# Performance work log

Measured on AMD Instinct MI355X. Metric: run time of the kernel, lower is better.

Reference implementation:

```python
import jax, jax.numpy as jnp
import numpy as np

B, S, D, H = 1, 4096, 1024, 16
HD = D // H  # 64
THETA = 10000.0


def precompute_freqs_cis(dim, end, theta=THETA):
    freqs = 1.0 / theta ** (np.arange(0, dim, 2, dtype=np.float32) / dim)  # [dim//2]
    t = np.arange(end, dtype=np.float32)
    f = np.outer(t, freqs)                       # [end, dim//2]
    f = np.concatenate((f, f), axis=-1)          # [end, dim]
    return jnp.asarray(np.cos(f), jnp.float32), jnp.asarray(np.sin(f), jnp.float32)


def rotate_half(x):
    x1 = x[..., : x.shape[-1] // 2]
    x2 = x[..., x.shape[-1] // 2:]
    return jnp.concatenate((-x2, x1), axis=-1)


def setup_inputs() -> dict:
    key = jax.random.key(0)
    ks = jax.random.split(key, 5)
    x = jax.random.normal(ks[0], (B, S, D), jnp.float32)
    scale = 0.02
    Wq = jax.random.normal(ks[1], (D, H, HD), jnp.float32) * scale
    Wk = jax.random.normal(ks[2], (D, H, HD), jnp.float32) * scale
    Wv = jax.random.normal(ks[3], (D, H, HD), jnp.float32) * scale
    Wo = jax.random.normal(ks[4], (H, HD, D), jnp.float32) * scale
    mask = jnp.tril(jnp.ones((S, S), jnp.bool_))[None, None]  # [1,1,S,S] causal
    return {"x": x, "mask": mask, "Wq": Wq, "Wk": Wk, "Wv": Wv, "Wo": Wo}


def reference(x, mask, Wq, Wk, Wv, Wo):
    # QKV projections: [B,S,D] x [D,H,HD] -> [B,S,H,HD]
    q = jnp.einsum('bsd,dhe->bshe', x, Wq)
    k = jnp.einsum('bsd,dhe->bshe', x, Wk)
    v = jnp.einsum('bsd,dhe->bshe', x, Wv)
    # Rotary position embedding
    cos, sin = precompute_freqs_cis(HD, S)
    cos = cos[None, :, None, :]  # [1,S,1,HD]
    sin = sin[None, :, None, :]
    q = q * cos + rotate_half(q) * sin
    k = k * cos + rotate_half(k) * sin
    # Scaled dot-product attention
    scale = 1.0 / jnp.sqrt(jnp.asarray(HD, jnp.float32))
    scores = jnp.einsum('bqhe,bkhe->bhqk', q * scale, k)  # [B,H,S,S]
    big_neg = jnp.finfo(scores.dtype).min
    scores = jnp.where(mask, scores, big_neg)
    attn = jax.nn.softmax(scores, axis=-1)
    ctx = jnp.einsum('bhqk,bkhe->bqhe', attn, v)  # [B,S,H,HD]
    # Output projection contracting (head, head_dim)
    out = jnp.einsum('bqhe,hed->bqd', ctx, Wo)  # [B,S,D]
    return out
```

## Files before the change

### kernel.cpp

```cpp
#include <hip/hip_runtime.h>
#include <hip/hip_bf16.h>
#include <stdint.h>
#include <stddef.h>

#define S_LEN 4096
#define DMODEL 1024
#define NHEAD 16
#define HDIM 64
#define L2E 1.4426950408889634f
#define FIXED_M 8.0f

typedef __attribute__((ext_vector_type(8))) short bf16x8;
typedef __attribute__((ext_vector_type(8))) unsigned short u16x8;
typedef __attribute__((ext_vector_type(4))) float f32x4;
typedef __attribute__((ext_vector_type(16))) float f32x16;

__device__ __forceinline__ unsigned short f2bf(float f) {
    unsigned int u = __float_as_uint(f);
    return (unsigned short)((u + 0x7FFFu + ((u >> 16) & 1u)) >> 16);
}
__device__ __forceinline__ float bf2f(unsigned short h) {
    return __uint_as_float(((unsigned int)h) << 16);
}

__device__ __forceinline__ void gload_lds16(const unsigned short* g, unsigned short* l) {
    __builtin_amdgcn_global_load_lds(
        (const __attribute__((address_space(1))) unsigned int*)g,
        (__attribute__((address_space(3))) unsigned int*)l, 16, 0, 0);
}

__global__ __launch_bounds__(256) void rope_table_kernel(float* __restrict__ ctab,
                                                         float* __restrict__ stab) {
    int i = blockIdx.x * 256 + threadIdx.x;
    int s = i >> 5, j = i & 31;
    float freq = exp2f(-0.41524101186092407f * (float)j);
    float ang = (float)s * freq;
    ctab[i] = cosf(ang);
    stab[i] = sinf(ang);
}

__global__ __launch_bounds__(256) void cvt_x_kernel(const float* __restrict__ x,
                                                    unsigned short* __restrict__ xb) {
    int i = (blockIdx.x * 256 + threadIdx.x) * 8;
    f32x4 a = *(const f32x4*)(x + i);
    f32x4 b = *(const f32x4*)(x + i + 4);
    u16x8 o;
    #pragma unroll
    for (int j = 0; j < 4; ++j) { o[j] = f2bf(a[j]); o[4 + j] = f2bf(b[j]); }
    *(u16x8*)(xb + i) = o;
}

__global__ __launch_bounds__(256) void cvt_wt_kernel(
    const float* __restrict__ w0, const float* __restrict__ w1,
    const float* __restrict__ w2, const float* __restrict__ w3,
    unsigned short* __restrict__ t0, unsigned short* __restrict__ t1,
    unsigned short* __restrict__ t2, unsigned short* __restrict__ t3) {
    const float* src; unsigned short* dst;
    switch (blockIdx.z) {
        case 0: src = w0; dst = t0; break;
        case 1: src = w1; dst = t1; break;
        case 2: src = w2; dst = t2; break;
        default: src = w3; dst = t3; break;
    }
    __shared__ float tile[64][65];
    int t = threadIdx.x;
    int k0 = blockIdx.y * 64, n0 = blockIdx.x * 64;
    int r = t >> 2, q4 = (t & 3) * 16;
    const float* sp = src + (size_t)(k0 + r) * DMODEL + n0 + q4;
    #pragma unroll
    for (int j = 0; j < 4; ++j) {
        f32x4 v = *(const f32x4*)(sp + j * 4);
        #pragma unroll
        for (int e = 0; e < 4; ++e) tile[r][q4 + j * 4 + e] = v[e];
    }
    __syncthreads();
    int n = t >> 2, kq = (t & 3) * 16;
    unsigned short* dp = dst + (size_t)(n0 + n) * DMODEL + k0 + kq;
    u16x8 a, b;
    #pragma unroll
    for (int j = 0; j < 8; ++j) { a[j] = f2bf(tile[kq + j][n]); b[j] = f2bf(tile[kq + 8 + j][n]); }
    *(u16x8*)dp = a;
    *(u16x8*)(dp + 8) = b;
}

template<int MODE>
__global__ __launch_bounds__(256) void gemm_kernel(
    const unsigned short* __restrict__ Ab,
    const unsigned short* __restrict__ B0,
    const unsigned short* __restrict__ B1,
    const unsigned short* __restrict__ B2,
    unsigned short* __restrict__ o0,
    unsigned short* __restrict__ o1,
    unsigned short* __restrict__ o2,
    float* __restrict__ fo,
    const float* __restrict__ ctab,
    const float* __restrict__ stab) {
    int z = blockIdx.z;
    const unsigned short* Bt = (MODE == 0) ? B0 : (z == 0 ? B0 : (z == 1 ? B1 : B2));
    unsigned short* outp     = (MODE == 0) ? o0 : (z == 0 ? o0 : (z == 1 ? o1 : o2));
    int m0 = blockIdx.y * 128, n0 = blockIdx.x * 128;
    __shared__ unsigned short As[128][64];
    __shared__ unsigned short Bs[128][64];
    int t = threadIdx.x, w = t >> 6, l = t & 63;
    int wm = w >> 1, wn = w & 1, g = l >> 4, c = l & 15;

    f32x4 acc[4][4];
    #pragma unroll
    for (int m = 0; m < 4; ++m)
        #pragma unroll
        for (int n = 0; n < 4; ++n) acc[m][n] = (f32x4){0.f, 0.f, 0.f, 0.f};

    int srow = l >> 3;
    int scol = (l & 7) * 8;

    for (int kt = 0; kt < DMODEL; kt += 64) {
        __syncthreads();
        #pragma unroll
        for (int ch = 0; ch < 4; ++ch) {
            int chunk = w + ch * 4;
            gload_lds16(Ab + (size_t)(m0 + chunk * 8 + srow) * DMODEL + kt + scol,
                        (unsigned short*)As + chunk * 512);
            gload_lds16(Bt + (size_t)(n0 + chunk * 8 + srow) * DMODEL + kt + scol,
                        (unsigned short*)Bs + chunk * 512);
        }
        __syncthreads();
        #pragma unroll
        for (int kk = 0; kk < 64; kk += 32) {
            bf16x8 af[4], bf[4];
            #pragma unroll
            for (int m = 0; m < 4; ++m) af[m] = *(const bf16x8*)&As[wm * 64 + m * 16 + c][kk + g * 8];
            #pragma unroll
            for (int n = 0; n < 4; ++n) bf[n] = *(const bf16x8*)&Bs[wn * 64 + n * 16 + c][kk + g * 8];
            #pragma unroll
            for (int m = 0; m < 4; ++m)
                #pragma unroll
                for (int n = 0; n < 4; ++n)
                    acc[m][n] = __builtin_amdgcn_mfma_f32_16x16x32_bf16(af[m], bf[n], acc[m][n], 0, 0, 0);
        }
    }

    if (MODE == 1 && z < 2) {
        float sc8 = (z == 0) ? 0.125f * L2E : 1.0f;
        #pragma unroll
        for (int m = 0; m < 4; ++m) {
            #pragma unroll
            for (int r = 0; r < 4; ++r) {
                int srw = m0 + wm * 64 + m * 16 + g * 4 + r;
                #pragma unroll
                for (int n = 0; n < 2; ++n) {
                    int e = n * 16 + c;
                    float cs = ctab[srw * 32 + e];
                    float sn = stab[srw * 32 + e];
                    float lo = acc[m][n][r], hi = acc[m][n + 2][r];
                    float nlo = (lo * cs - hi * sn) * sc8;
                    float nhi = (hi * cs + lo * sn) * sc8;
                    size_t base = (size_t)srw * DMODEL + n0 + wn * 64;
                    outp[base + n * 16 + c]       = f2bf(nlo);
                    outp[base + (n + 2) * 16 + c] = f2bf(nhi);
                }
            }
        }
    } else if (MODE == 1) {
        #pragma unroll
        for (int m = 0; m < 4; ++m)
            #pragma unroll
            for (int r = 0; r < 4; ++r) {
                int srw = m0 + wm * 64 + m * 16 + g * 4 + r;
                size_t base = (size_t)srw * DMODEL + n0 + wn * 64;
                #pragma unroll
                for (int n = 0; n < 4; ++n)
                    outp[base + n * 16 + c] = f2bf(acc[m][n][r]);
            }
    } else {
        #pragma unroll
        for (int m = 0; m < 4; ++m)
            #pragma unroll
            for (int r = 0; r < 4; ++r) {
                int srw = m0 + wm * 64 + m * 16 + g * 4 + r;
                size_t base = (size_t)srw * DMODEL + n0 + wn * 64;
                #pragma unroll
                for (int n = 0; n < 4; ++n)
                    fo[base + n * 16 + c] = acc[m][n][r];
            }
    }
}

__global__ __launch_bounds__(512, 4) void attn_kernel(
    const unsigned short* __restrict__ q,
    const unsigned short* __restrict__ k,
    const unsigned short* __restrict__ v,
    unsigned short* __restrict__ Opart,
    float* __restrict__ lpart) {
    int h = blockIdx.x;
    int qb = 31 - (int)blockIdx.y;
    int p = blockIdx.z;
    int t = threadIdx.x, w = t >> 6, l = t & 63, c = l & 31, hi = l >> 5;
    int rg = w & 3, ks = w >> 2;

    __shared__ __align__(16) char smraw[36864];
    unsigned short (*KsT)[64][72] = (unsigned short (*)[64][72])smraw;
    unsigned short (*VtT)[64][72] = (unsigned short (*)[64][72])(smraw + 18432);
    float (*Om)[32][64] = (float (*)[32][64])smraw;
    float* ml           = (float*)(smraw + 32768);

    int qrow = qb * 128 + rg * 32 + c;
    int wrmax = qb * 128 + rg * 32 + 31;

    bf16x8 qf[4];
    {
        const unsigned short* qp = q + (size_t)qrow * DMODEL + h * HDIM + hi * 8;
        #pragma unroll
        for (int s = 0; s < 4; ++s) qf[s] = *(const bf16x8*)(qp + s * 16);
    }

    f32x16 o0, o1;
    #pragma unroll
    for (int i = 0; i < 16; ++i) { o0[i] = 0.f; o1[i] = 0.f; }
    float lsum = 0.f;

    int ts = t & 255;
    int skr = ts >> 2, skc = (ts & 3) * 16;
    int svr = ts & 63, svc = ((ts >> 6) & 3) * 16;
    const unsigned short* gkb = k + (size_t)skr * DMODEL + h * HDIM + skc;
    const unsigned short* gvb = v + (size_t)svr * DMODEL + h * HDIM + svc;

    int NIT = (qb + 2) >> 1;
    int tb = p * (qb + 1);
    u16x8 ka, kb, va, vb;
    if (ks <= qb) {
        size_t off = (size_t)((tb + ks) * 64) * DMODEL;
        ka = *(const u16x8*)(gkb + off);
        kb = *(const u16x8*)(gkb + off + 8);
        va = *(const u16x8*)(gvb + off);
        vb = *(const u16x8*)(gvb + off + 8);
        *(u16x8*)&KsT[ks][skr][skc]     = ka;
        *(u16x8*)&KsT[ks][skr][skc + 8] = kb;
        #pragma unroll
        for (int j = 0; j < 8; ++j) {
            VtT[ks][svc + j][svr]     = va[j];
            VtT[ks][svc + 8 + j][svr] = vb[j];
        }
    }

    for (int it = 0; it < NIT; ++it) {
        int j = 2 * it + ks;
        int kv0 = (tb + j) * 64;
        if (j + 2 <= qb) {
            size_t off = (size_t)(kv0 + 128) * DMODEL;
            ka = *(const u16x8*)(gkb + off);
            kb = *(const u16x8*)(gkb + off + 8);
            va = *(const u16x8*)(gvb + off);
            vb = *(const u16x8*)(gvb + off + 8);
        }
        __syncthreads();

        if (j <= qb) {
            #pragma unroll
            for (int h2 = 0; h2 < 2; ++h2) {
                int kbase = kv0 + h2 * 32;
                if (kbase > wrmax) continue;

                f32x16 sf;
                #pragma unroll
                for (int i = 0; i < 16; ++i) sf[i] = 0.f;
                __builtin_amdgcn_s_setprio(1);
                #pragma unroll
                for (int s = 0; s < 4; ++s) {
                    bf16x8 kf = *(const bf16x8*)&KsT[ks][h2 * 32 + c][s * 16 + hi * 8];
                    sf = __builtin_amdgcn_mfma_f32_32x32x16_bf16(kf, qf[s], sf, 0, 0, 0);
                }
                __builtin_amdgcn_s_setprio(0);

                if (kbase + 31 >= wrmax) {
                    #pragma unroll
                    for (int r = 0; r < 16; ++r) {
                        int key = kbase + (r & 3) + 8 * (r >> 2) + 4 * hi;
                        if (key > qrow) sf[r] = -3.0e38f;
                    }
                }

                float ps = 0.f;
                unsigned int dw[8];
                #pragma unroll
                for (int jj = 0; jj < 8; ++jj) {
                    float p0 = exp2f(sf[2 * jj]     - FIXED_M);
                    float p1 = exp2f(sf[2 * jj + 1] - FIXED_M);
                    unsigned int u0 = __float_as_uint(p0) & 0xFFFF0000u;
                    unsigned int u1 = __float_as_uint(p1) & 0xFFFF0000u;
                    ps += __uint_as_float(u0) + __uint_as_float(u1);
                    dw[jj] = (u0 >> 16) | u1;
                }
                ps += __shfl_xor(ps, 32, 64);
                lsum += ps;

                {
                    auto r0 = __builtin_amdgcn_permlane32_swap(dw[0], dw[2], false, false);
                    dw[0] = r0[0]; dw[2] = r0[1];
                    auto r1 = __builtin_amdgcn_permlane32_swap(dw[1], dw[3], false, false);
                    dw[1] = r1[0]; dw[3] = r1[1];
                    auto r2 = __builtin_amdgcn_permlane32_swap(dw[4], dw[6], false, false);
                    dw[4] = r2[0]; dw[6] = r2[1];
                    auto r3 = __builtin_amdgcn_permlane32_swap(dw[5], dw[7], false, false);
                    dw[5] = r3[0]; dw[7] = r3[1];
                }
                union { unsigned int u[8]; bf16x8 v[2]; } pu;
                #pragma unroll
                for (int jj = 0; jj < 8; ++jj) pu.u[jj] = dw[jj];

                __builtin_amdgcn_s_setprio(1);
                {
                    bf16x8 vf00 = *(const bf16x8*)&VtT[ks][c][h2 * 32 + hi * 8];
                    bf16x8 vf01 = *(const bf16x8*)&VtT[ks][c][h2 * 32 + 16 + hi * 8];
                    bf16x8 vf10 = *(const bf16x8*)&VtT[ks][32 + c][h2 * 32 + hi * 8];
                    bf16x8 vf11 = *(const bf16x8*)&VtT[ks][32 + c][h2 * 32 + 16 + hi * 8];
                    o0 = __builtin_amdgcn_mfma_f32_32x32x16_bf16(pu.v[0], vf00, o0, 0, 0, 0);
                    o0 = __builtin_amdgcn_mfma_f32_32x32x16_bf16(pu.v[1], vf01, o0, 0, 0, 0);
                    o1 = __builtin_amdgcn_mfma_f32_32x32x16_bf16(pu.v[0], vf10, o1, 0, 0, 0);
                    o1 = __builtin_amdgcn_mfma_f32_32x32x16_bf16(pu.v[1], vf11, o1, 0, 0, 0);
                }
                __builtin_amdgcn_s_setprio(0);
            }
        }

        if (it + 1 < NIT) {
            __syncthreads();
            if (j + 2 <= qb) {
                *(u16x8*)&KsT[ks][skr][skc]     = ka;
                *(u16x8*)&KsT[ks][skr][skc + 8] = kb;
                #pragma unroll
                for (int jj = 0; jj < 8; ++jj) {
                    VtT[ks][svc + jj][svr]     = va[jj];
                    VtT[ks][svc + 8 + jj][svr] = vb[jj];
                }
            }
        }
    }

    __syncthreads();
    if (ks == 0) {
        #pragma unroll
        for (int r = 0; r < 16; ++r) {
            int rl = (r & 3) + 8 * (r >> 2) + 4 * hi;
            Om[rg][rl][c]      = o0[r];
            Om[rg][rl][c + 32] = o1[r];
        }
        if (hi == 0) ml[(rg << 5) + c] = lsum;
    }
    __syncthreads();
    if (ks == 1) {
        float lc = ml[(rg << 5) + c] + lsum;
        #pragma unroll
        for (int r = 0; r < 16; ++r) {
            int rl = (r & 3) + 8 * (r >> 2) + 4 * hi;
            int grow = qb * 128 + rg * 32 + rl;
            size_t ob = ((size_t)(p * 16 + h) * 4096 + grow) * 64 + c;
            Opart[ob]      = f2bf(Om[rg][rl][c]      + o0[r]);
            Opart[ob + 32] = f2bf(Om[rg][rl][c + 32] + o1[r]);
        }
        if (hi == 0)
            lpart[(size_t)(p * 16 + h) * 4096 + qrow] = lc;
    }
}

__global__ __launch_bounds__(256) void attn_merge_kernel(
    const unsigned short* __restrict__ Op,
    const float* __restrict__ lp,
    unsigned short* __restrict__ ctx) {
    int i = blockIdx.x * 256 + threadIdx.x;
    int g8 = i & 7;
    int row = (i >> 3) & 4095;
    int h = i >> 15;
    size_t idx = (size_t)h * 4096 + row;
    const size_t PS = (size_t)16 * 4096;
    float inv = 1.0f / (lp[idx] + lp[PS + idx]);
    u16x8 v0 = *(const u16x8*)(Op + idx * 64 + g8 * 8);
    u16x8 v1 = *(const u16x8*)(Op + (PS + idx) * 64 + g8 * 8);
    u16x8 o;
    #pragma unroll
    for (int j = 0; j < 8; ++j)
        o[j] = f2bf((bf2f(v0[j]) + bf2f(v1[j])) * inv);
    *(u16x8*)(ctx + (size_t)row * DMODEL + h * 64 + g8 * 8) = o;
}

extern "C" void kernel_launch(void* const* d_in, const int* in_sizes, int n_in,
                              void* d_out, int out_size, void* d_ws, size_t ws_size,
                              hipStream_t stream) {
    const float* x  = (const float*)d_in[0];
    const float* Wq = (const float*)d_in[2];
    const float* Wk = (const float*)d_in[3];
    const float* Wv = (const float*)d_in[4];
    const float* Wo = (const float*)d_in[5];

    char* ws = (char*)d_ws;
    float* ctab = (float*)(ws);
    float* stab = (float*)(ws + (512u << 10));
    unsigned short* ctx = (unsigned short*)(ws + (1u  << 20));
    unsigned short* Wtq = (unsigned short*)(ws + (1u  << 20));
    unsigned short* Wtk = (unsigned short*)(ws + (3u  << 20));
    unsigned short* Wtv = (unsigned short*)(ws + (5u  << 20));
    unsigned short* Wto = (unsigned short*)(ws + (9u  << 20));
    unsigned short* kr  = (unsigned short*)(ws + (11u << 20));
    unsigned short* vb  = (unsigned short*)(ws + (19u << 20));
    unsigned short* qr  = (unsigned short*)(ws + (27u << 20));
    unsigned short* xb  = (unsigned short*)(ws + (35u << 20));
    unsigned short* Opart = (unsigned short*)(ws + (43u << 20));
    float* lpart = (float*)(ws + (59u << 20));

    rope_table_kernel<<<(S_LEN * 32) / 256, 256, 0, stream>>>(ctab, stab);
    cvt_x_kernel<<<(S_LEN * DMODEL) / 2048, 256, 0, stream>>>(x, xb);
    cvt_wt_kernel<<<dim3(16, 16, 4), 256, 0, stream>>>(Wq, Wk, Wv, Wo, Wtq, Wtk, Wtv, Wto);
    gemm_kernel<1><<<dim3(8, 32, 3), 256, 0, stream>>>(xb, Wtq, Wtk, Wtv,
                                                       qr, kr, vb, nullptr, ctab, stab);
    attn_kernel<<<dim3(16, 32, 2), 512, 0, stream>>>(qr, kr, vb, Opart, lpart);
    attn_merge_kernel<<<(16 * 4096 * 8) / 256, 256, 0, stream>>>(Opart, lpart, ctx);
    gemm_kernel<0><<<dim3(8, 32, 1), 256, 0, stream>>>(ctx, Wto, nullptr, nullptr,
                                                       nullptr, nullptr, nullptr,
                                                       (float*)d_out, ctab, stab);
}
```

Baseline: 176.9 us.

## Use padded LDS with register-staged loads in GEMM; round softmax probabilities

Result: faster. 172.0 us (-2.7%).

```diff
diff --git a/kernel.cpp b/kernel.cpp
--- a/kernel.cpp
+++ b/kernel.cpp
@@ -21,12 +21,6 @@
 }
 __device__ __forceinline__ float bf2f(unsigned short h) {
     return __uint_as_float(((unsigned int)h) << 16);
-}
-
-__device__ __forceinline__ void gload_lds16(const unsigned short* g, unsigned short* l) {
-    __builtin_amdgcn_global_load_lds(
-        (const __attribute__((address_space(1))) unsigned int*)g,
-        (__attribute__((address_space(3))) unsigned int*)l, 16, 0, 0);
 }
 
 __global__ __launch_bounds__(256) void rope_table_kernel(float* __restrict__ ctab,
@@ -99,8 +93,8 @@
     const unsigned short* Bt = (MODE == 0) ? B0 : (z == 0 ? B0 : (z == 1 ? B1 : B2));
     unsigned short* outp     = (MODE == 0) ? o0 : (z == 0 ? o0 : (z == 1 ? o1 : o2));
     int m0 = blockIdx.y * 128, n0 = blockIdx.x * 128;
-    __shared__ unsigned short As[128][64];
-    __shared__ unsigned short Bs[128][64];
+    __shared__ unsigned short As[128][72];
+    __shared__ unsigned short Bs[128][72];
     int t = threadIdx.x, w = t >> 6, l = t & 63;
     int wm = w >> 1, wn = w & 1, g = l >> 4, c = l & 15;
 
@@ -110,18 +104,21 @@
         #pragma unroll
         for (int n = 0; n < 4; ++n) acc[m][n] = (f32x4){0.f, 0.f, 0.f, 0.f};
 
-    int srow = l >> 3;
-    int scol = (l & 7) * 8;
+    int sr = t >> 1, scc = (t & 1) * 32;
 
     for (int kt = 0; kt < DMODEL; kt += 64) {
         __syncthreads();
-        #pragma unroll
-        for (int ch = 0; ch < 4; ++ch) {
-            int chunk = w + ch * 4;
-            gload_lds16(Ab + (size_t)(m0 + chunk * 8 + srow) * DMODEL + kt + scol,
-                        (unsigned short*)As + chunk * 512);
-            gload_lds16(Bt + (size_t)(n0 + chunk * 8 + srow) * DMODEL + kt + scol,
-                        (unsigned short*)Bs + chunk * 512);
+        {
+            const unsigned short* gp = Ab + (size_t)(m0 + sr) * DMODEL + kt + scc;
+            #pragma unroll
+            for (int j = 0; j < 4; ++j)
+                *(u16x8*)&As[sr][scc + j * 8] = *(const u16x8*)(gp + j * 8);
+        }
+        {
+            const unsigned short* gp = Bt + (size_t)(n0 + sr) * DMODEL + kt + scc;
+            #pragma unroll
+            for (int j = 0; j < 4; ++j)
+                *(u16x8*)&Bs[sr][scc + j * 8] = *(const u16x8*)(gp + j * 8);
         }
         __syncthreads();
         #pragma unroll
@@ -145,16 +142,16 @@
         for (int m = 0; m < 4; ++m) {
             #pragma unroll
             for (int r = 0; r < 4; ++r) {
-                int srw = m0 + wm * 64 + m * 16 + g * 4 + r;
+                int srow = m0 + wm * 64 + m * 16 + g * 4 + r;
                 #pragma unroll
                 for (int n = 0; n < 2; ++n) {
                     int e = n * 16 + c;
-                    float cs = ctab[srw * 32 + e];
-                    float sn = stab[srw * 32 + e];
+                    float cs = ctab[srow * 32 + e];
+                    float sn = stab[srow * 32 + e];
                     float lo = acc[m][n][r], hi = acc[m][n + 2][r];
                     float nlo = (lo * cs - hi * sn) * sc8;
                     float nhi = (hi * cs + lo * sn) * sc8;
-                    size_t base = (size_t)srw * DMODEL + n0 + wn * 64;
+                    size_t base = (size_t)srow * DMODEL + n0 + wn * 64;
                     outp[base + n * 16 + c]       = f2bf(nlo);
                     outp[base + (n + 2) * 16 + c] = f2bf(nhi);
                 }
@@ -165,8 +162,8 @@
         for (int m = 0; m < 4; ++m)
             #pragma unroll
             for (int r = 0; r < 4; ++r) {
-                int srw = m0 + wm * 64 + m * 16 + g * 4 + r;
-                size_t base = (size_t)srw * DMODEL + n0 + wn * 64;
+                int srow = m0 + wm * 64 + m * 16 + g * 4 + r;
+                size_t base = (size_t)srow * DMODEL + n0 + wn * 64;
                 #pragma unroll
                 for (int n = 0; n < 4; ++n)
                     outp[base + n * 16 + c] = f2bf(acc[m][n][r]);
@@ -176,8 +173,8 @@
         for (int m = 0; m < 4; ++m)
             #pragma unroll
             for (int r = 0; r < 4; ++r) {
-                int srw = m0 + wm * 64 + m * 16 + g * 4 + r;
-                size_t base = (size_t)srw * DMODEL + n0 + wn * 64;
+                int srow = m0 + wm * 64 + m * 16 + g * 4 + r;
+                size_t base = (size_t)srow * DMODEL + n0 + wn * 64;
                 #pragma unroll
                 for (int n = 0; n < 4; ++n)
                     fo[base + n * 16 + c] = acc[m][n][r];
@@ -285,12 +282,12 @@
                 for (int jj = 0; jj < 8; ++jj) {
                     float p0 = exp2f(sf[2 * jj]     - FIXED_M);
                     float p1 = exp2f(sf[2 * jj + 1] - FIXED_M);
-                    unsigned int u0 = __float_as_uint(p0) & 0xFFFF0000u;
-                    unsigned int u1 = __float_as_uint(p1) & 0xFFFF0000u;
-                    ps += __uint_as_float(u0) + __uint_as_float(u1);
-                    dw[jj] = (u0 >> 16) | u1;
-                }
-                ps += __shfl_xor(ps, 32, 64);
+                    ps += p0 + p1;
+                    union { struct { __hip_bfloat16 x, y; } h; unsigned int u; } cv;
+                    cv.h.x = __float2bfloat16(p0);
+                    cv.h.y = __float2bfloat16(p1);
+                    dw[jj] = cv.u;
+                }
                 lsum += ps;
 
                 {
@@ -335,6 +332,8 @@
             }
         }
     }
+
+    lsum += __shfl_xor(lsum, 32, 64);
 
     __syncthreads();
     if (ks == 0) {
```
